# Performance work log

Hardware: AMD Instinct MI355X
Metric: run time of the kernel (lower is better)

## Reference

```python
import jax, jax.numpy as jnp
import numpy as np

E = 1024   # embed_size
H = 16     # heads
D = E // H # head_dim = 64
F = 4 * E  # ffn hidden = 4096
N, S = 4, 2048
EPS = 1e-5


def _layernorm(x, w, b):
    m = jnp.mean(x, axis=-1, keepdims=True)
    v = jnp.var(x, axis=-1, keepdims=True)
    return (x - m) * jax.lax.rsqrt(v + EPS) * w + b


def setup_inputs() -> dict:
    key = jax.random.key(0)
    ks = jax.random.split(key, 10)
    s = 0.02
    return {
        "x": jax.random.normal(ks[0], (N, S, E), dtype=jnp.float32),
        "Wq": jax.random.normal(ks[1], (E, E), dtype=jnp.float32) * s,
        "Wk": jax.random.normal(ks[2], (E, E), dtype=jnp.float32) * s,
        "Wv": jax.random.normal(ks[3], (E, E), dtype=jnp.float32) * s,
        "Wo": jax.random.normal(ks[4], (E, E), dtype=jnp.float32) * s,
        "bo": jnp.zeros((E,), dtype=jnp.float32),
        "ln1_w": jnp.ones((E,), dtype=jnp.float32),
        "ln1_b": jnp.zeros((E,), dtype=jnp.float32),
        "ln2_w": jnp.ones((E,), dtype=jnp.float32),
        "ln2_b": jnp.zeros((E,), dtype=jnp.float32),
        "W1": jax.random.normal(ks[5], (F, E), dtype=jnp.float32) * s,
        "bf1": jnp.zeros((F,), dtype=jnp.float32),
        "W2": jax.random.normal(ks[6], (E, F), dtype=jnp.float32) * s,
        "bf2": jnp.zeros((E,), dtype=jnp.float32),
    }


def reference(x, Wq, Wk, Wv, Wo, bo, ln1_w, ln1_b, ln2_w, ln2_b, W1, bf1, W2, bf2):
    n, s, _ = x.shape
    # projections (torch Linear: x @ W.T), no bias for q/k/v
    q = (x @ Wq.T).reshape(n, s, H, D).transpose(0, 2, 1, 3)  # (N,H,S,D)
    k = (x @ Wk.T).reshape(n, s, H, D).transpose(0, 2, 1, 3)
    v = (x @ Wv.T).reshape(n, s, H, D).transpose(0, 2, 1, 3)
    # NOTE: faithful to original einsum strings applied to permuted tensors.
    # energy: (N, H, H, S)
    energy = jnp.einsum('nqhd,nkhd->nqkh', q, k)
    attention = jax.nn.softmax(energy / jnp.sqrt(jnp.float32(D)), axis=3)
    # out: (N, H, S, D); k and v axes each summed independently (as in torch)
    out = jnp.einsum('nqkh,nvhd->nqhd', attention, v).reshape(n, s, E)
    attn = out @ Wo.T + bo
    # residual + LN1 (dropout is identity in eval mode)
    x = _layernorm(attn + x, ln1_w, ln1_b)
    # FFN
    ff = jnp.maximum(x @ W1.T + bf1, 0.0) @ W2.T + bf2
    x = _layernorm(ff + x, ln2_w, ln2_b)
    return x
```

## Files before the change

### kernel.cpp

```cpp
#include <hip/hip_runtime.h>

typedef __attribute__((ext_vector_type(8))) __bf16 bf16x8;
typedef __attribute__((ext_vector_type(8))) unsigned short us8;
typedef __attribute__((ext_vector_type(4))) float f32x4;

#define DEV __device__ __forceinline__

DEV unsigned short f2bf(float f) {
    unsigned u = __builtin_bit_cast(unsigned, f);
    u += 0x7fffu + ((u >> 16) & 1u);
    return (unsigned short)(u >> 16);
}
DEV float bf2f(unsigned short h) {
    return __builtin_bit_cast(float, (unsigned)h << 16);
}

DEV void gload_lds16(const void* g, void* l) {
    __builtin_amdgcn_global_load_lds(
        (const __attribute__((address_space(1))) unsigned int*)g,
        (__attribute__((address_space(3))) unsigned int*)l, 16, 0, 0);
}

template <int EPI>
__global__ __launch_bounds__(256, 2) void gemm_bt(
    const unsigned short* __restrict__ A, const unsigned short* __restrict__ B,
    void* __restrict__ Cv, const float* __restrict__ bias, int M, int N, int K) {
    __shared__ __attribute__((aligned(16))) unsigned short As[128 * 64];
    __shared__ __attribute__((aligned(16))) unsigned short Bs[128 * 64];
    const int tid = threadIdx.x;
    const int m0 = blockIdx.y * 128;
    const int n0 = blockIdx.x * 128;
    const int wave = tid >> 6;
    const int wr = (wave >> 1) * 64, wc = (wave & 1) * 64;
    const int r = tid & 15;
    const int g = (tid >> 4) & 3;

    f32x4 acc[4][4] = {};
    const unsigned short* Ag = A + (size_t)m0 * K;
    const unsigned short* Bg = B + (size_t)n0 * K;

    for (int k0 = 0; k0 < K; k0 += 64) {
#pragma unroll
        for (int c = 0; c < 4; ++c) {
            int e = c * 2048 + tid * 8;
            int row = e >> 6, col = e & 63;
            gload_lds16(Ag + row * K + (k0 + col), (char*)As + e * 2);
            gload_lds16(Bg + row * K + (k0 + col), (char*)Bs + e * 2);
        }
        __syncthreads();
#pragma unroll
        for (int kk = 0; kk < 2; ++kk) {
            bf16x8 av[4], bv[4];
#pragma unroll
            for (int i = 0; i < 4; ++i)
                av[i] = *(const bf16x8*)(As + (wr + i * 16 + r) * 64 + kk * 32 + g * 8);
#pragma unroll
            for (int i = 0; i < 4; ++i)
                bv[i] = *(const bf16x8*)(Bs + (wc + i * 16 + r) * 64 + kk * 32 + g * 8);
#pragma unroll
            for (int mi = 0; mi < 4; ++mi)
#pragma unroll
                for (int ni = 0; ni < 4; ++ni)
                    acc[mi][ni] = __builtin_amdgcn_mfma_f32_16x16x32_bf16(
                        av[mi], bv[ni], acc[mi][ni], 0, 0, 0);
        }
        __syncthreads();
    }

    const int crow0 = m0 + wr + g * 4;
    const int ccol0 = n0 + wc + r;
#pragma unroll
    for (int mi = 0; mi < 4; ++mi) {
#pragma unroll
        for (int ni = 0; ni < 4; ++ni) {
            int col = ccol0 + ni * 16;
            float bval = (EPI == 2) ? bias[col] : 0.f;
#pragma unroll
            for (int j = 0; j < 4; ++j) {
                int row = crow0 + mi * 16 + j;
                float v = acc[mi][ni][j];
                if (EPI == 0) {
                    ((unsigned short*)Cv)[(size_t)row * N + col] = f2bf(v);
                } else if (EPI == 1) {
                    ((float*)Cv)[(size_t)row * N + col] = v;
                } else {
                    v = fmaxf(v + bval, 0.f);
                    ((unsigned short*)Cv)[(size_t)row * N + col] = f2bf(v);
                }
            }
        }
    }
}

__global__ __launch_bounds__(256) void cvt_kernel(
    const float* __restrict__ in, unsigned short* __restrict__ out, int n4) {
    int idx = blockIdx.x * 256 + threadIdx.x;
    if (idx >= n4) return;
    float4 v = *(const float4*)(in + (size_t)idx * 4);
    ushort4 u = make_ushort4(f2bf(v.x), f2bf(v.y), f2bf(v.z), f2bf(v.w));
    *(ushort4*)(out + (size_t)idx * 4) = u;
}

__global__ __launch_bounds__(256) void energy_kernel(
    const unsigned short* __restrict__ QKV, float* __restrict__ E) {
    __shared__ __attribute__((aligned(16))) unsigned short Qs[8 * 1024];
    __shared__ __attribute__((aligned(16))) unsigned short Ks[8 * 1024];
    const int tid = threadIdx.x;
    const int n = blockIdx.y;
    const int s0 = blockIdx.x * 8;
#pragma unroll
    for (int c = 0; c < 4; ++c) {
        int e = c * 2048 + tid * 8;
        int row = e >> 10, col = e & 1023;
        int jj = col >> 6, db = (col >> 3) & 7;
        int sw = jj * 64 + (((db + jj) & 7) << 3);
        size_t gbase = (size_t)(n * 2048 + s0 + row) * 3072;
        *(us8*)(Qs + row * 1024 + sw) = *(const us8*)(QKV + gbase + col);
        *(us8*)(Ks + row * 1024 + sw) = *(const us8*)(QKV + gbase + 1024 + col);
    }
    __syncthreads();
    const int i = tid >> 4, j = tid & 15;
#pragma unroll
    for (int s = 0; s < 8; ++s) {
        float acc = 0.f;
#pragma unroll
        for (int d8 = 0; d8 < 8; ++d8) {
            us8 q = *(const us8*)(Qs + s * 1024 + i * 64 + (((d8 + i) & 7) << 3));
            us8 k = *(const us8*)(Ks + s * 1024 + j * 64 + (((d8 + j) & 7) << 3));
#pragma unroll
            for (int t = 0; t < 8; ++t) acc += bf2f(q[t]) * bf2f(k[t]);
        }
        E[(size_t)(n * 2048 + s0 + s) * 256 + tid] = acc * 0.125f;
    }
}

__global__ __launch_bounds__(256) void smax_part(
    const float* __restrict__ E, float* __restrict__ Mp, float* __restrict__ Zp) {
    const int p = threadIdx.x, n = blockIdx.y, sc = blockIdx.x;
    float m = -1e30f, z = 0.f;
    const float* base = E + ((size_t)n * 2048 + sc * 128) * 256 + p;
    for (int s = 0; s < 128; ++s) {
        float e = base[(size_t)s * 256];
        float mn = fmaxf(m, e);
        z = z * __expf(m - mn) + __expf(e - mn);
        m = mn;
    }
    int idx = (n * 16 + sc) * 256 + p;
    Mp[idx] = m;
    Zp[idx] = z;
}

__global__ __launch_bounds__(256) void smax_fin(
    const float* __restrict__ Mp, const float* __restrict__ Zp,
    float* __restrict__ Mf, float* __restrict__ RZf) {
    const int p = threadIdx.x, n = blockIdx.x;
    float m = -1e30f;
    for (int c = 0; c < 16; ++c) m = fmaxf(m, Mp[(n * 16 + c) * 256 + p]);
    float z = 0.f;
    for (int c = 0; c < 16; ++c)
        z += Zp[(n * 16 + c) * 256 + p] * __expf(Mp[(n * 16 + c) * 256 + p] - m);
    Mf[n * 256 + p] = m;
    RZf[n * 256 + p] = 1.f / z;
}

__global__ __launch_bounds__(256) void attnsrc_kernel(
    const unsigned short* __restrict__ QKV, const float* __restrict__ E,
    const float* __restrict__ Mf, const float* __restrict__ RZf,
    unsigned short* __restrict__ ASRC) {
    const int lane = threadIdx.x & 63;
    const int widx = blockIdx.x * 4 + (threadIdx.x >> 6);
    const int n = widx >> 11, s = widx & 2047;
    float vs = 0.f;
    const unsigned short* vrow = QKV + (size_t)(n * 2048 + s) * 3072 + 2048;
#pragma unroll
    for (int h = 0; h < 16; ++h) vs += bf2f(vrow[h * 64 + lane]);
    float aval = 0.f;
    if (lane < 16) {
        const float* erow = E + (size_t)(n * 2048 + s) * 256 + lane * 16;
        const float* mrow = Mf + n * 256 + lane * 16;
        const float* zrow = RZf + n * 256 + lane * 16;
#pragma unroll
        for (int j = 0; j < 16; ++j)
            aval += __expf(erow[j] - mrow[j]) * zrow[j];
    }
#pragma unroll
    for (int h = 0; h < 16; ++h) {
        float ah = __shfl(aval, h, 64);
        size_t row = (size_t)n * 2048 + h * 128 + (s >> 4);
        ASRC[row * 1024 + (s & 15) * 64 + lane] = f2bf(ah * vs);
    }
}

__global__ __launch_bounds__(256) void ln_kernel(
    const float* __restrict__ lin, const float* __restrict__ bias,
    const float* __restrict__ resid, const float* __restrict__ w,
    const float* __restrict__ b, unsigned short* __restrict__ obf,
    float* __restrict__ of) {
    __shared__ float sm[16];
    const int row = blockIdx.x, c = threadIdx.x * 4;
    const size_t off = (size_t)row * 1024 + c;
    float4 v = *(const float4*)(lin + off);
    float4 bs = *(const float4*)(bias + c);
    float4 rx = *(const float4*)(resid + off);
    float t0 = v.x + bs.x + rx.x;
    float t1 = v.y + bs.y + rx.y;
    float t2 = v.z + bs.z + rx.z;
    float t3 = v.w + bs.w + rx.w;
    float s = t0 + t1 + t2 + t3;
    float ss = t0 * t0 + t1 * t1 + t2 * t2 + t3 * t3;
#pragma unroll
    for (int o = 32; o > 0; o >>= 1) {
        s += __shfl_down(s, o, 64);
        ss += __shfl_down(ss, o, 64);
    }
    const int wv = threadIdx.x >> 6, ln = threadIdx.x & 63;
    if (ln == 0) {
        sm[wv] = s;
        sm[8 + wv] = ss;
    }
    __syncthreads();
    if (threadIdx.x == 0) {
        sm[4] = sm[0] + sm[1] + sm[2] + sm[3];
        sm[12] = sm[8] + sm[9] + sm[10] + sm[11];
    }
    __syncthreads();
    s = sm[4];
    ss = sm[12];
    float mean = s * (1.f / 1024.f);
    float var = ss * (1.f / 1024.f) - mean * mean;
    float rstd = rsqrtf(var + 1e-5f);
    float4 wv4 = *(const float4*)(w + c);
    float4 bv4 = *(const float4*)(b + c);
    float o0 = (t0 - mean) * rstd * wv4.x + bv4.x;
    float o1 = (t1 - mean) * rstd * wv4.y + bv4.y;
    float o2 = (t2 - mean) * rstd * wv4.z + bv4.z;
    float o3 = (t3 - mean) * rstd * wv4.w + bv4.w;
    if (of) {
        float4 o = make_float4(o0, o1, o2, o3);
        *(float4*)(of + off) = o;
    }
    if (obf) {
        ushort4 u = make_ushort4(f2bf(o0), f2bf(o1), f2bf(o2), f2bf(o3));
        *(ushort4*)(obf + off) = u;
    }
}

extern "C" void kernel_launch(void* const* d_in, const int* in_sizes, int n_in,
                              void* d_out, int out_size, void* d_ws, size_t ws_size,
                              hipStream_t stream) {
    const float* x = (const float*)d_in[0];
    const float* Wq = (const float*)d_in[1];
    const float* Wk = (const float*)d_in[2];
    const float* Wv = (const float*)d_in[3];
    const float* Wo = (const float*)d_in[4];
    const float* bo = (const float*)d_in[5];
    const float* ln1w = (const float*)d_in[6];
    const float* ln1b = (const float*)d_in[7];
    const float* ln2w = (const float*)d_in[8];
    const float* ln2b = (const float*)d_in[9];
    const float* W1 = (const float*)d_in[10];
    const float* bf1 = (const float*)d_in[11];
    const float* W2 = (const float*)d_in[12];
    const float* bf2 = (const float*)d_in[13];

    char* ws = (char*)d_ws;
    const size_t MB = 1u << 20;
    unsigned short* W1bf = (unsigned short*)(ws + 0);
    unsigned short* W2bf = (unsigned short*)(ws + 8 * MB);
    unsigned short* x1bf = (unsigned short*)(ws + 16 * MB);
    float* x1f = (float*)(ws + 32 * MB);
    float* ffb = (float*)(ws + 64 * MB);
    unsigned short* xbf = (unsigned short*)(ws + 96 * MB);
    unsigned short* Wqkvbf = (unsigned short*)(ws + 112 * MB);
    unsigned short* Wobf = (unsigned short*)(ws + 118 * MB);
    unsigned short* QKV = (unsigned short*)(ws + 120 * MB);
    float* EN = (float*)(ws + 168 * MB);
    float* Mp = (float*)(ws + 176 * MB);
    float* Zp = (float*)(ws + 176 * MB + 128 * 1024);
    float* Mfin = (float*)(ws + 176 * MB + 256 * 1024);
    float* RZfin = (float*)(ws + 176 * MB + 272 * 1024);
    unsigned short* ASRC = (unsigned short*)(ws + 177 * MB);
    float* ALIN = (float*)(ws + 120 * MB);
    unsigned short* H1 = (unsigned short*)(ws + 96 * MB);

    auto cvt = [&](const float* src, unsigned short* dst, int n) {
        int n4 = n >> 2;
        cvt_kernel<<<dim3((n4 + 255) / 256), dim3(256), 0, stream>>>(src, dst, n4);
    };
    cvt(x, xbf, 8192 * 1024);
    cvt(Wq, Wqkvbf, 1024 * 1024);
    cvt(Wk, Wqkvbf + 1024 * 1024, 1024 * 1024);
    cvt(Wv, Wqkvbf + 2 * 1024 * 1024, 1024 * 1024);
    cvt(Wo, Wobf, 1024 * 1024);
    cvt(W1, W1bf, 4096 * 1024);
    cvt(W2, W2bf, 4096 * 1024);

    gemm_bt<0><<<dim3(24, 64), 256, 0, stream>>>(xbf, Wqkvbf, QKV, nullptr, 8192, 3072, 1024);
    energy_kernel<<<dim3(256, 4), 256, 0, stream>>>(QKV, EN);
    smax_part<<<dim3(16, 4), 256, 0, stream>>>(EN, Mp, Zp);
    smax_fin<<<dim3(4), 256, 0, stream>>>(Mp, Zp, Mfin, RZfin);
    attnsrc_kernel<<<dim3(2048), 256, 0, stream>>>(QKV, EN, Mfin, RZfin, ASRC);
    gemm_bt<1><<<dim3(8, 64), 256, 0, stream>>>(ASRC, Wobf, ALIN, nullptr, 8192, 1024, 1024);
    ln_kernel<<<dim3(8192), 256, 0, stream>>>(ALIN, bo, x, ln1w, ln1b, x1bf, x1f);
    gemm_bt<2><<<dim3(32, 64), 256, 0, stream>>>(x1bf, W1bf, H1, bf1, 8192, 4096, 1024);
    gemm_bt<1><<<dim3(8, 64), 256, 0, stream>>>(H1, W2bf, ffb, nullptr, 8192, 1024, 4096);
    ln_kernel<<<dim3(8192), 256, 0, stream>>>(ffb, bf2, x1f, ln2w, ln2b, nullptr, (float*)d_out);
}
```

Before: 482.0 us.

## Replace GEMM with 256x256 double-buffered swizzled kernel and split-K for narrow GEMMs

```diff
diff --git a/kernel.cpp b/kernel.cpp
--- a/kernel.cpp
+++ b/kernel.cpp
@@ -21,56 +21,118 @@
         (__attribute__((address_space(3))) unsigned int*)l, 16, 0, 0);
 }
 
+#define VMCNT8 asm volatile("s_waitcnt vmcnt(8)" ::: "memory")
+#define VMCNT0 asm volatile("s_waitcnt vmcnt(0)" ::: "memory")
+#define BAR __builtin_amdgcn_s_barrier()
+
 template <int EPI>
-__global__ __launch_bounds__(256, 2) void gemm_bt(
+__global__ __launch_bounds__(512) void gemm256(
     const unsigned short* __restrict__ A, const unsigned short* __restrict__ B,
-    void* __restrict__ Cv, const float* __restrict__ bias, int M, int N, int K) {
-    __shared__ __attribute__((aligned(16))) unsigned short As[128 * 64];
-    __shared__ __attribute__((aligned(16))) unsigned short Bs[128 * 64];
-    const int tid = threadIdx.x;
-    const int m0 = blockIdx.y * 128;
-    const int n0 = blockIdx.x * 128;
-    const int wave = tid >> 6;
-    const int wr = (wave >> 1) * 64, wc = (wave & 1) * 64;
-    const int r = tid & 15;
-    const int g = (tid >> 4) & 3;
-
-    f32x4 acc[4][4] = {};
-    const unsigned short* Ag = A + (size_t)m0 * K;
-    const unsigned short* Bg = B + (size_t)n0 * K;
-
-    for (int k0 = 0; k0 < K; k0 += 64) {
-#pragma unroll
-        for (int c = 0; c < 4; ++c) {
-            int e = c * 2048 + tid * 8;
-            int row = e >> 6, col = e & 63;
-            gload_lds16(Ag + row * K + (k0 + col), (char*)As + e * 2);
-            gload_lds16(Bg + row * K + (k0 + col), (char*)Bs + e * 2);
+    void* __restrict__ Cv, const float* __restrict__ bias,
+    int lda, int ldb, int N, int Kslice) {
+    extern __shared__ char smem[];
+    const int t = threadIdx.x;
+    const int m0 = blockIdx.y * 256;
+    const int n0 = blockIdx.x * 256;
+    const int z = blockIdx.z;
+    const unsigned short* Ag = A + (size_t)z * Kslice;
+    const unsigned short* Bg = B + (size_t)z * Kslice;
+    const int NT = Kslice >> 6;
+
+    size_t aoff[4], boff[4];
+    int ldb_off[4];
+#pragma unroll
+    for (int j = 0; j < 4; ++j) {
+        int cj = j * 512 + t;
+        int row = cj >> 3, slot = cj & 7;
+        int col = (slot ^ (row & 7)) << 3;
+        aoff[j] = (size_t)(m0 + row) * lda + col;
+        boff[j] = (size_t)(n0 + row) * ldb + col;
+        ldb_off[j] = cj << 4;
+    }
+
+    const int lane = t & 63, r = lane & 15, g = lane >> 4;
+    const int wid = t >> 6, wm = wid >> 2, wn = wid & 3;
+    const int s0 = (g ^ (r & 7)) << 4;
+    const int aRow = (wm * 128 + r) * 128;
+    const int bRow = (wn * 64 + r) * 128;
+
+#define LDA8(base, mi, kk) \
+    (*(const bf16x8*)((base) + aRow + (mi) * 2048 + (s0 ^ ((kk) << 6))))
+#define LDB8(base, ni, kk) \
+    (*(const bf16x8*)((base) + 32768 + bRow + (ni) * 2048 + (s0 ^ ((kk) << 6))))
+
+#define STAGE(base, kt)                                                       \
+    do {                                                                      \
+        const unsigned short* _as = Ag + (size_t)(kt) * 64;                   \
+        const unsigned short* _bs = Bg + (size_t)(kt) * 64;                   \
+        _Pragma("unroll") for (int j = 0; j < 4; ++j)                         \
+            gload_lds16(_as + aoff[j], (base) + ldb_off[j]);                  \
+        _Pragma("unroll") for (int j = 0; j < 4; ++j)                         \
+            gload_lds16(_bs + boff[j], (base) + 32768 + ldb_off[j]);          \
+    } while (0)
+
+#define PHASE_BODY(MH)                                                        \
+    BAR;                                                                      \
+    asm volatile("s_waitcnt lgkmcnt(0)" ::: "memory");                        \
+    __builtin_amdgcn_sched_barrier(0);                                        \
+    __builtin_amdgcn_s_setprio(1);                                            \
+    _Pragma("unroll") for (int q = 0; q < 4; ++q)                             \
+        _Pragma("unroll") for (int ni = 0; ni < 4; ++ni)                      \
+            acc[(MH) * 4 + q][ni] = __builtin_amdgcn_mfma_f32_16x16x32_bf16(  \
+                af[q], bfr[ni], acc[(MH) * 4 + q][ni], 0, 0, 0);              \
+    __builtin_amdgcn_s_setprio(0);
+
+#define COMPUTE_TILE(base)                                                    \
+    do {                                                                      \
+        _Pragma("unroll") for (int kk = 0; kk < 2; ++kk) {                    \
+            bf16x8 bfr[4], af[4];                                             \
+            _Pragma("unroll") for (int ni = 0; ni < 4; ++ni)                  \
+                bfr[ni] = LDB8(base, ni, kk);                                 \
+            _Pragma("unroll") for (int q = 0; q < 4; ++q)                     \
+                af[q] = LDA8(base, q, kk);                                    \
+            PHASE_BODY(0)                                                     \
+            BAR;                                                              \
+            _Pragma("unroll") for (int q = 0; q < 4; ++q)                     \
+                af[q] = LDA8(base, 4 + q, kk);                                \
+            PHASE_BODY(1)                                                     \
+        }                                                                     \
+        BAR;                                                                  \
+    } while (0)
+
+    f32x4 acc[8][4] = {};
+    char* buf0 = smem;
+    char* buf1 = smem + 65536;
+
+    STAGE(buf0, 0);
+    STAGE(buf1, 1);
+    VMCNT8;
+    BAR;
+
+    for (int kt = 0; kt < NT; kt += 2) {
+        COMPUTE_TILE(buf0);
+        if (kt + 2 < NT) {
+            STAGE(buf0, kt + 2);
+            VMCNT8;
+        } else {
+            VMCNT0;
         }
-        __syncthreads();
-#pragma unroll
-        for (int kk = 0; kk < 2; ++kk) {
-            bf16x8 av[4], bv[4];
-#pragma unroll
-            for (int i = 0; i < 4; ++i)
-                av[i] = *(const bf16x8*)(As + (wr + i * 16 + r) * 64 + kk * 32 + g * 8);
-#pragma unroll
-            for (int i = 0; i < 4; ++i)
-                bv[i] = *(const bf16x8*)(Bs + (wc + i * 16 + r) * 64 + kk * 32 + g * 8);
-#pragma unroll
-            for (int mi = 0; mi < 4; ++mi)
-#pragma unroll
-                for (int ni = 0; ni < 4; ++ni)
-                    acc[mi][ni] = __builtin_amdgcn_mfma_f32_16x16x32_bf16(
-                        av[mi], bv[ni], acc[mi][ni], 0, 0, 0);
+        BAR;
+        COMPUTE_TILE(buf1);
+        if (kt + 3 < NT) {
+            STAGE(buf1, kt + 3);
+            VMCNT8;
+        } else {
+            VMCNT0;
         }
-        __syncthreads();
-    }
-
-    const int crow0 = m0 + wr + g * 4;
-    const int ccol0 = n0 + wc + r;
-#pragma unroll
-    for (int mi = 0; mi < 4; ++mi) {
+        BAR;
+    }
+
+    const int crow0 = m0 + wm * 128 + g * 4;
+    const int ccol0 = n0 + wn * 64 + r;
+    float* Cp = (float*)Cv + (size_t)gridDim.y * 256 * N * z;
+#pragma unroll
+    for (int mi = 0; mi < 8; ++mi) {
 #pragma unroll
         for (int ni = 0; ni < 4; ++ni) {
             int col = ccol0 + ni * 16;
@@ -82,7 +144,7 @@
                 if (EPI == 0) {
                     ((unsigned short*)Cv)[(size_t)row * N + col] = f2bf(v);
                 } else if (EPI == 1) {
-                    ((float*)Cv)[(size_t)row * N + col] = v;
+                    Cp[(size_t)row * N + col] = v;
                 } else {
                     v = fmaxf(v + bval, 0.f);
                     ((unsigned short*)Cv)[(size_t)row * N + col] = f2bf(v);
@@ -90,6 +152,11 @@
             }
         }
     }
+#undef LDA8
+#undef LDB8
+#undef STAGE
+#undef PHASE_BODY
+#undef COMPUTE_TILE
 }
 
 __global__ __launch_bounds__(256) void cvt_kernel(
@@ -192,10 +259,10 @@
 }
 
 __global__ __launch_bounds__(256) void ln_kernel(
-    const float* __restrict__ lin, const float* __restrict__ bias,
-    const float* __restrict__ resid, const float* __restrict__ w,
-    const float* __restrict__ b, unsigned short* __restrict__ obf,
-    float* __restrict__ of) {
+    const float* __restrict__ lin, const float* __restrict__ lin2,
+    const float* __restrict__ bias, const float* __restrict__ resid,
+    const float* __restrict__ w, const float* __restrict__ b,
+    unsigned short* __restrict__ obf, float* __restrict__ of) {
     __shared__ float sm[16];
     const int row = blockIdx.x, c = threadIdx.x * 4;
     const size_t off = (size_t)row * 1024 + c;
@@ -206,6 +273,10 @@
     float t1 = v.y + bs.y + rx.y;
     float t2 = v.z + bs.z + rx.z;
     float t3 = v.w + bs.w + rx.w;
+    if (lin2) {
+        float4 v2 = *(const float4*)(lin2 + off);
+        t0 += v2.x; t1 += v2.y; t2 += v2.z; t3 += v2.w;
+    }
     float s = t0 + t1 + t2 + t3;
     float ss = t0 * t0 + t1 * t1 + t2 * t2 + t3 * t3;
 #pragma unroll
@@ -267,21 +338,26 @@
     const size_t MB = 1u << 20;
     unsigned short* W1bf = (unsigned short*)(ws + 0);
     unsigned short* W2bf = (unsigned short*)(ws + 8 * MB);
-    unsigned short* x1bf = (unsigned short*)(ws + 16 * MB);
-    float* x1f = (float*)(ws + 32 * MB);
-    float* ffb = (float*)(ws + 64 * MB);
-    unsigned short* xbf = (unsigned short*)(ws + 96 * MB);
-    unsigned short* Wqkvbf = (unsigned short*)(ws + 112 * MB);
-    unsigned short* Wobf = (unsigned short*)(ws + 118 * MB);
-    unsigned short* QKV = (unsigned short*)(ws + 120 * MB);
-    float* EN = (float*)(ws + 168 * MB);
-    float* Mp = (float*)(ws + 176 * MB);
-    float* Zp = (float*)(ws + 176 * MB + 128 * 1024);
-    float* Mfin = (float*)(ws + 176 * MB + 256 * 1024);
-    float* RZfin = (float*)(ws + 176 * MB + 272 * 1024);
-    unsigned short* ASRC = (unsigned short*)(ws + 177 * MB);
-    float* ALIN = (float*)(ws + 120 * MB);
-    unsigned short* H1 = (unsigned short*)(ws + 96 * MB);
+    unsigned short* Wobf = (unsigned short*)(ws + 16 * MB);
+    unsigned short* Wqkvbf = (unsigned short*)(ws + 18 * MB);
+    float* Mp = (float*)(ws + 24 * MB);
+    float* Zp = (float*)(ws + 24 * MB + 64 * 1024);
+    float* Mfin = (float*)(ws + 24 * MB + 128 * 1024);
+    float* RZfin = (float*)(ws + 24 * MB + 160 * 1024);
+    float* x1f = (float*)(ws + 16 * MB);
+    unsigned short* ASRC = (unsigned short*)(ws + 48 * MB);
+    unsigned short* x1bf = (unsigned short*)(ws + 48 * MB);
+    float* AL = (float*)(ws + 64 * MB);
+    unsigned short* H1 = (unsigned short*)(ws + 64 * MB);
+    unsigned short* QKV = (unsigned short*)(ws + 128 * MB);
+    float* FF = (float*)(ws + 128 * MB);
+    unsigned short* xbf = (unsigned short*)(ws + 176 * MB);
+    float* EN = (float*)(ws + 176 * MB);
+
+    auto k0 = gemm256<0>; auto k1 = gemm256<1>; auto k2 = gemm256<2>;
+    (void)hipFuncSetAttribute((const void*)k0, hipFuncAttributeMaxDynamicSharedMemorySize, 131072);
+    (void)hipFuncSetAttribute((const void*)k1, hipFuncAttributeMaxDynamicSharedMemorySize, 131072);
+    (void)hipFuncSetAttribute((const void*)k2, hipFuncAttributeMaxDynamicSharedMemorySize, 131072);
 
     auto cvt = [&](const float* src, unsigned short* dst, int n) {
         int n4 = n >> 2;
@@ -295,14 +371,20 @@
     cvt(W1, W1bf, 4096 * 1024);
     cvt(W2, W2bf, 4096 * 1024);
 
-    gemm_bt<0><<<dim3(24, 64), 256, 0, stream>>>(xbf, Wqkvbf, QKV, nullptr, 8192, 3072, 1024);
+    gemm256<0><<<dim3(12, 32, 1), 512, 131072, stream>>>(
+        xbf, Wqkvbf, QKV, nullptr, 1024, 1024, 3072, 1024);
     energy_kernel<<<dim3(256, 4), 256, 0, stream>>>(QKV, EN);
     smax_part<<<dim3(16, 4), 256, 0, stream>>>(EN, Mp, Zp);
     smax_fin<<<dim3(4), 256, 0, stream>>>(Mp, Zp, Mfin, RZfin);
     attnsrc_kernel<<<dim3(2048), 256, 0, stream>>>(QKV, EN, Mfin, RZfin, ASRC);
-    gemm_bt<1><<<dim3(8, 64), 256, 0, stream>>>(ASRC, Wobf, ALIN, nullptr, 8192, 1024, 1024);
-    ln_kernel<<<dim3(8192), 256, 0, stream>>>(ALIN, bo, x, ln1w, ln1b, x1bf, x1f);
-    gemm_bt<2><<<dim3(32, 64), 256, 0, stream>>>(x1bf, W1bf, H1, bf1, 8192, 4096, 1024);
-    gemm_bt<1><<<dim3(8, 64), 256, 0, stream>>>(H1, W2bf, ffb, nullptr, 8192, 1024, 4096);
-    ln_kernel<<<dim3(8192), 256, 0, stream>>>(ffb, bf2, x1f, ln2w, ln2b, nullptr, (float*)d_out);
-}
+    gemm256<1><<<dim3(4, 32, 2), 512, 131072, stream>>>(
+        ASRC, Wobf, AL, nullptr, 1024, 1024, 1024, 512);
+    ln_kernel<<<dim3(8192), 256, 0, stream>>>(
+        AL, AL + (size_t)8192 * 1024, bo, x, ln1w, ln1b, x1bf, x1f);
+    gemm256<2><<<dim3(16, 32, 1), 512, 131072, stream>>>(
+        x1bf, W1bf, H1, bf1, 1024, 1024, 4096, 1024);
+    gemm256<1><<<dim3(4, 32, 2), 512, 131072, stream>>>(
+        H1, W2bf, FF, nullptr, 4096, 4096, 1024, 2048);
+    ln_kernel<<<dim3(8192), 256, 0, stream>>>(
+        FF, FF + (size_t)8192 * 1024, bf2, x1f, ln2w, ln2b, nullptr, (float*)d_out);
+}
```

After: 460.8 us. 4.4% less time.
